# Kernel tuning notes

Hardware: AMD Instinct MI355X
Metric: run time of the kernel (lower is better)

Reference implementation:

```python
import jax, jax.numpy as jnp
import numpy as np

N_NODES, N_EDGES = 50000, 800000
IN, HID, HEADS, OUT = 128, 64, 4, 64


def _segment_softmax(e, seg, n):
    # softmax over edges grouped by source node (torch.sparse.softmax dim=1), per head
    m = jax.ops.segment_max(e, seg, num_segments=n)
    ex = jnp.exp(e - m[seg])
    s = jax.ops.segment_sum(ex, seg, num_segments=n)
    return ex / s[seg]


def _attention_layer(x, src, dst, lw, lb, aw, ab, final):
    n = x.shape[0]
    h = jax.nn.leaky_relu(x @ lw.T + lb, 0.2)            # (N, F)
    f = h.shape[1]
    # Faithful decomposition of Conv1d(2*F*H, H, k=1, groups=H) applied to
    # concat([tile(h_i, H), tile(h_j, H)]): group k covers tiled copies 2k and 2k+1;
    # copies < H come from h_i (src), copies >= H from h_j (dst).
    k = jnp.arange(HEADS)
    sel1 = (2 * k < HEADS).astype(h.dtype)[:, None]       # first half of group weights
    sel2 = (2 * k + 1 < HEADS).astype(h.dtype)[:, None]   # second half
    Wi = aw[:, :f] * sel1 + aw[:, f:] * sel2              # (H, F) acting on h_src
    Wj = aw[:, :f] * (1.0 - sel1) + aw[:, f:] * (1.0 - sel2)  # (H, F) acting on h_dst
    e = (h @ Wi.T)[src] + (h @ Wj.T)[dst] + ab            # (E, H)
    alpha = _segment_softmax(e, src, n)                   # (E, H)
    # h2[i] = sum_{j in N(i)} h[j] outer alpha[ij]  -> (N, F, H)
    h2 = jax.ops.segment_sum(h[dst][:, :, None] * alpha[:, None, :], src, num_segments=n)
    if final:
        return jax.nn.relu(h2.mean(axis=-1))              # (N, OUT)
    return jax.nn.relu(h2.reshape(n, -1))                 # (N, F*H)


def setup_inputs() -> dict:
    key = jax.random.key(0)
    ks = jax.random.split(key, 16)
    d = {}
    d["x"] = jax.random.normal(ks[0], (N_NODES, IN), jnp.float32)
    dims_in = [IN, HID * HEADS, HID * HEADS]
    dims_out = [HID, HID, OUT]
    i = 1
    for L in range(3):
        di, do = dims_in[L], dims_out[L]
        d[f"lin{L}_w"] = jax.random.normal(ks[i], (do, di), jnp.float32) / np.float32(np.sqrt(di)); i += 1
        d[f"lin{L}_b"] = jax.random.normal(ks[i], (do,), jnp.float32) * 0.01; i += 1
        d[f"att{L}_w"] = jax.random.normal(ks[i], (HEADS, 2 * do), jnp.float32) / np.float32(np.sqrt(2 * do)); i += 1
        d[f"att{L}_b"] = jax.random.normal(ks[i], (HEADS,), jnp.float32) * 0.01; i += 1
    d["src"] = jnp.sort(jax.random.randint(ks[13], (N_EDGES,), 0, N_NODES, dtype=jnp.int32))
    d["dst"] = jax.random.randint(ks[14], (N_EDGES,), 0, N_NODES, dtype=jnp.int32)
    return d


def reference(x, lin0_w, lin0_b, att0_w, att0_b, lin1_w, lin1_b, att1_w, att1_b,
              lin2_w, lin2_b, att2_w, att2_b, src, dst):
    layers = [(lin0_w, lin0_b, att0_w, att0_b),
              (lin1_w, lin1_b, att1_w, att1_b),
              (lin2_w, lin2_b, att2_w, att2_b)]
    out = x
    for i, (lw, lb, aw, ab) in enumerate(layers):
        out = _attention_layer(out, src, dst, lw, lb, aw, ab, final=(i == len(layers) - 1))
    return out
```

## Files before the change

kernel.cpp:

```cpp
#include <hip/hip_runtime.h>
#include <hip/hip_fp16.h>

#define N_NODES 50000
#define N_EDGES 800000

typedef _Float16 half8 __attribute__((ext_vector_type(8)));
typedef _Float16 f16x4 __attribute__((ext_vector_type(4)));
typedef float floatx4 __attribute__((ext_vector_type(4)));

__global__ __launch_bounds__(256) void setup_kernel(const int* __restrict__ src,
                                                    int* __restrict__ row_ptr,
                                                    const float* __restrict__ lw0,
                                                    const float* __restrict__ lw1,
                                                    const float* __restrict__ lw2,
                                                    _Float16* __restrict__ w0p,
                                                    _Float16* __restrict__ w1p,
                                                    _Float16* __restrict__ w2p) {
    int idx = blockIdx.x * 256 + threadIdx.x;
    if (blockIdx.y == 0) {
        if (idx > N_NODES) return;
        int lo = 0, hi = N_EDGES;
        while (lo < hi) {
            int mid = (lo + hi) >> 1;
            if (src[mid] < idx) lo = mid + 1; else hi = mid;
        }
        row_ptr[idx] = lo;
        return;
    }
    if (blockIdx.y == 1) {
        if (idx < 64 * 128) w0p[idx] = (_Float16)lw0[idx];
        return;
    }
    if (idx >= 64 * 192) return;
    int o = idx / 192, r = idx % 192;
    int ch = r >> 6, f = r & 63;
    const float* lw = (blockIdx.y == 2) ? lw1 : lw2;
    float v;
    if (ch == 0)      v = lw[o * 256 + f * 4 + 0] + lw[o * 256 + f * 4 + 1];
    else if (ch == 1) v = lw[o * 256 + f * 4 + 2];
    else              v = lw[o * 256 + f * 4 + 3];
    (blockIdx.y == 2 ? w1p : w2p)[idx] = (_Float16)v;
}

template <typename TIn, int K>
__global__ __launch_bounds__(256) void lin_kernel(const TIn* __restrict__ in,
                                                  const _Float16* __restrict__ w,
                                                  const float* __restrict__ b,
                                                  const float* __restrict__ aw,
                                                  _Float16* __restrict__ h,
                                                  float2* __restrict__ s, int n) {
    const int t = threadIdx.x;
    const int l = t & 63;
    const int wv = t >> 6;
    const int arow = l & 15;
    const int kg = l >> 4;
    const long rowbase = (long)blockIdx.x * 64 + wv * 16;
    long arow_g = rowbase + arow;
    if (arow_g >= n) arow_g = n - 1;

    floatx4 acc[4] = {};

    for (int kc = 0; kc < K; kc += 32) {
        const int ks = kc + kg * 8;
        half8 a;
        if (sizeof(TIn) == 4) {
            const TIn* ap = in + arow_g * K + ks;
            #pragma unroll
            for (int j = 0; j < 8; ++j) a[j] = (_Float16)ap[j];
        } else {
            a = *(const half8*)((const _Float16*)in + arow_g * K + ks);
        }
        #pragma unroll
        for (int ct = 0; ct < 4; ++ct) {
            half8 bb = *(const half8*)(w + (long)(ct * 16 + arow) * K + ks);
            acc[ct] = __builtin_amdgcn_mfma_f32_16x16x32_f16(a, bb, acc[ct], 0, 0, 0);
        }
    }

    const int c = l & 15;
    const int rq = l >> 4;
    float bias[4], a2c[4], a3c[4];
    #pragma unroll
    for (int ct = 0; ct < 4; ++ct) {
        int col = ct * 16 + c;
        bias[ct] = b[col];
        a2c[ct] = aw[2 * 128 + col] + aw[2 * 128 + 64 + col];
        a3c[ct] = aw[3 * 128 + col] + aw[3 * 128 + 64 + col];
    }
    #pragma unroll
    for (int r = 0; r < 4; ++r) {
        long row = rowbase + rq * 4 + r;
        bool ok = row < n;
        float q2 = 0.f, q3 = 0.f;
        _Float16 hv[4];
        #pragma unroll
        for (int ct = 0; ct < 4; ++ct) {
            float u = acc[ct][r] + bias[ct];
            u = u > 0.f ? u : 0.2f * u;
            q2 += u * a2c[ct];
            q3 += u * a3c[ct];
            hv[ct] = (_Float16)u;
        }
        if (ok) {
            #pragma unroll
            for (int ct = 0; ct < 4; ++ct) h[row * 64 + ct * 16 + c] = hv[ct];
        }
        #pragma unroll
        for (int o = 1; o < 16; o <<= 1) {
            q2 += __shfl_xor(q2, o);
            q3 += __shfl_xor(q3, o);
        }
        if (c == 0 && ok) s[row] = make_float2(__expf(q2), __expf(q3));
    }
}

template <int FINAL>
__global__ __launch_bounds__(256) void layer_kernel(const _Float16* __restrict__ hfeat,
                                                    const float2* __restrict__ E,
                                                    const int* __restrict__ dst,
                                                    const int* __restrict__ row_ptr,
                                                    const _Float16* __restrict__ w,
                                                    const float* __restrict__ b,
                                                    const float* __restrict__ aw,
                                                    _Float16* __restrict__ h_out,
                                                    float2* __restrict__ s_out,
                                                    float* __restrict__ out_f) {
    __shared__ _Float16 g_lds[16][200];
    __shared__ float2 spart[4][16];

    const int t = threadIdx.x;
    const int l = t & 63;
    const int wv = t >> 6;
    const int q = l >> 4;
    const int fl = l & 15;
    const int base = blockIdx.x * 16;
    const int i = base + wv * 4 + q;

    const int r0 = row_ptr[i];
    const int deg = row_ptr[i + 1] - r0;
    int md = deg;
    md = max(md, __shfl_xor(md, 16));
    md = max(md, __shfl_xor(md, 32));

    float am[4] = {}, a2[4] = {}, a3[4] = {};
    float S2 = 0.f, S3 = 0.f;
    const int safew = deg > 0 ? r0 + deg - 1 : 0;

    for (int c0 = 0; c0 < md; c0 += 16) {
        const int dl = dst[min(r0 + c0 + fl, safew)];
        const int jn = min(16, md - c0);
        for (int j = 0; j < jn; j += 4) {
            int dg[4]; float vm[4];
            #pragma unroll
            for (int g = 0; g < 4; ++g) {
                const int sl = j + g;
                dg[g] = __shfl(dl, (q << 4) | sl);
                vm[g] = (c0 + sl < deg) ? 1.f : 0.f;
            }
            f16x4 hv[4]; float2 Ev[4];
            #pragma unroll
            for (int g = 0; g < 4; ++g) {
                hv[g] = *(const f16x4*)(hfeat + (long)dg[g] * 64 + fl * 4);
                Ev[g] = E[dg[g]];
            }
            #pragma unroll
            for (int g = 0; g < 4; ++g) {
                const float e2 = vm[g] * Ev[g].x, e3 = vm[g] * Ev[g].y;
                S2 += e2; S3 += e3;
                #pragma unroll
                for (int k = 0; k < 4; ++k) {
                    const float hf = (float)hv[g][k];
                    am[k] += vm[g] * hf;
                    a2[k] += e2 * hf;
                    a3[k] += e3 * hf;
                }
            }
        }
    }

    const float inv_deg = deg > 0 ? 1.f / (float)deg : 0.f;
    const float i2 = deg > 0 ? 1.f / S2 : 0.f;
    const float i3 = deg > 0 ? 1.f / S3 : 0.f;

    if (FINAL) {
        floatx4 o;
        #pragma unroll
        for (int k = 0; k < 4; ++k)
            o[k] = fmaxf(0.5f * inv_deg * am[k] + 0.25f * (a2[k] * i2 + a3[k] * i3), 0.f);
        *(floatx4*)(out_f + (long)i * 64 + fl * 4) = o;
        return;
    }

    {
        const int nl = wv * 4 + q;
        f16x4 o0, o1, o2;
        #pragma unroll
        for (int k = 0; k < 4; ++k) {
            o0[k] = (_Float16)fmaxf(am[k] * inv_deg, 0.f);
            o1[k] = (_Float16)fmaxf(a2[k] * i2, 0.f);
            o2[k] = (_Float16)fmaxf(a3[k] * i3, 0.f);
        }
        *(f16x4*)(&g_lds[nl][fl * 4])       = o0;
        *(f16x4*)(&g_lds[nl][64 + fl * 4])  = o1;
        *(f16x4*)(&g_lds[nl][128 + fl * 4]) = o2;
    }
    __syncthreads();

    floatx4 acc = {};
    #pragma unroll
    for (int kc = 0; kc < 192; kc += 32) {
        const int ks = kc + q * 8;
        half8 a = *(const half8*)(&g_lds[fl][ks]);
        half8 bb = *(const half8*)(w + (long)(wv * 16 + fl) * 192 + ks);
        acc = __builtin_amdgcn_mfma_f32_16x16x32_f16(a, bb, acc, 0, 0, 0);
    }

    const int col = wv * 16 + fl;
    const float bias = b[col];
    const float a2c = aw[2 * 128 + col] + aw[2 * 128 + 64 + col];
    const float a3c = aw[3 * 128 + col] + aw[3 * 128 + 64 + col];
    #pragma unroll
    for (int r = 0; r < 4; ++r) {
        const int row = q * 4 + r;
        float u = acc[r] + bias;
        u = u > 0.f ? u : 0.2f * u;
        h_out[(long)(base + row) * 64 + col] = (_Float16)u;
        float q2 = u * a2c, q3 = u * a3c;
        #pragma unroll
        for (int o = 1; o < 16; o <<= 1) {
            q2 += __shfl_xor(q2, o);
            q3 += __shfl_xor(q3, o);
        }
        if (fl == 0) spart[wv][row] = make_float2(q2, q3);
    }
    __syncthreads();
    if (t < 16) {
        const float2 p0 = spart[0][t], p1 = spart[1][t], p2 = spart[2][t], p3 = spart[3][t];
        s_out[base + t] = make_float2(__expf(p0.x + p1.x + p2.x + p3.x),
                                      __expf(p0.y + p1.y + p2.y + p3.y));
    }
}

extern "C" void kernel_launch(void* const* d_in, const int* in_sizes, int n_in,
                              void* d_out, int out_size, void* d_ws, size_t ws_size,
                              hipStream_t stream) {
    const float* x = (const float*)d_in[0];
    const float* lw[3] = {(const float*)d_in[1], (const float*)d_in[5], (const float*)d_in[9]};
    const float* lb[3] = {(const float*)d_in[2], (const float*)d_in[6], (const float*)d_in[10]};
    const float* aw[3] = {(const float*)d_in[3], (const float*)d_in[7], (const float*)d_in[11]};
    const int* src = (const int*)d_in[13];
    const int* dst = (const int*)d_in[14];
    float* out = (float*)d_out;

    const int N = N_NODES;

    _Float16* hA = (_Float16*)d_ws;
    _Float16* hB = hA + (size_t)N * 64;
    float2* sA = (float2*)(hB + (size_t)N * 64);
    float2* sB = sA + N;
    _Float16* w0p = (_Float16*)(sB + N);
    _Float16* w1p = w0p + 64 * 128;
    _Float16* w2p = w1p + 64 * 192;
    int* row_ptr = (int*)(w2p + 64 * 192);

    const int lin_grid = (N + 63) / 64;
    const int layer_grid = N / 16;

    setup_kernel<<<dim3(196, 4), 256, 0, stream>>>(src, row_ptr, lw[0], lw[1], lw[2],
                                                   w0p, w1p, w2p);

    lin_kernel<float, 128><<<lin_grid, 256, 0, stream>>>(x, w0p, lb[0], aw[0], hA, sA, N);

    layer_kernel<0><<<layer_grid, 256, 0, stream>>>(hA, sA, dst, row_ptr,
                                                    w1p, lb[1], aw[1], hB, sB, out);

    layer_kernel<0><<<layer_grid, 256, 0, stream>>>(hB, sB, dst, row_ptr,
                                                    w2p, lb[2], aw[2], hA, sA, out);

    layer_kernel<1><<<layer_grid, 256, 0, stream>>>(hA, sA, dst, row_ptr,
                                                    w2p, lb[2], aw[2], hB, sB, out);
}
```

Baseline: 199.9 us.

## Fuse all stages into one cooperative persistent kernel with grid syncs

Replaces the five separate launches (setup, linear, three layer kernels) with one cooperative kernel of 768 blocks. The blocks loop over virtual blocks and use grid-wide syncs between stages, falling back to separate launches if the cooperative launch fails. The aim is to remove launch gaps and tail effects between dependent stages. In exchange, the grid is capped at 768 persistent blocks, the setup work now runs as a grid-stride loop, and grid.sync barriers cost time of their own.

```diff
diff --git a/kernel.cpp b/kernel.cpp
--- a/kernel.cpp
+++ b/kernel.cpp
@@ -1,60 +1,31 @@
 #include <hip/hip_runtime.h>
 #include <hip/hip_fp16.h>
+#include <hip/hip_cooperative_groups.h>
+
+namespace cg = cooperative_groups;
 
 #define N_NODES 50000
 #define N_EDGES 800000
+#define COOP_GRID 768
 
 typedef _Float16 half8 __attribute__((ext_vector_type(8)));
 typedef _Float16 f16x4 __attribute__((ext_vector_type(4)));
 typedef float floatx4 __attribute__((ext_vector_type(4)));
 
-__global__ __launch_bounds__(256) void setup_kernel(const int* __restrict__ src,
-                                                    int* __restrict__ row_ptr,
-                                                    const float* __restrict__ lw0,
-                                                    const float* __restrict__ lw1,
-                                                    const float* __restrict__ lw2,
-                                                    _Float16* __restrict__ w0p,
-                                                    _Float16* __restrict__ w1p,
-                                                    _Float16* __restrict__ w2p) {
-    int idx = blockIdx.x * 256 + threadIdx.x;
-    if (blockIdx.y == 0) {
-        if (idx > N_NODES) return;
-        int lo = 0, hi = N_EDGES;
-        while (lo < hi) {
-            int mid = (lo + hi) >> 1;
-            if (src[mid] < idx) lo = mid + 1; else hi = mid;
-        }
-        row_ptr[idx] = lo;
-        return;
-    }
-    if (blockIdx.y == 1) {
-        if (idx < 64 * 128) w0p[idx] = (_Float16)lw0[idx];
-        return;
-    }
-    if (idx >= 64 * 192) return;
-    int o = idx / 192, r = idx % 192;
-    int ch = r >> 6, f = r & 63;
-    const float* lw = (blockIdx.y == 2) ? lw1 : lw2;
-    float v;
-    if (ch == 0)      v = lw[o * 256 + f * 4 + 0] + lw[o * 256 + f * 4 + 1];
-    else if (ch == 1) v = lw[o * 256 + f * 4 + 2];
-    else              v = lw[o * 256 + f * 4 + 3];
-    (blockIdx.y == 2 ? w1p : w2p)[idx] = (_Float16)v;
-}
 
 template <typename TIn, int K>
-__global__ __launch_bounds__(256) void lin_kernel(const TIn* __restrict__ in,
-                                                  const _Float16* __restrict__ w,
-                                                  const float* __restrict__ b,
-                                                  const float* __restrict__ aw,
-                                                  _Float16* __restrict__ h,
-                                                  float2* __restrict__ s, int n) {
-    const int t = threadIdx.x;
+__device__ __forceinline__ void lin_body(int vb, int t,
+                                         const TIn* __restrict__ in,
+                                         const _Float16* __restrict__ w,
+                                         const float* __restrict__ b,
+                                         const float* __restrict__ aw,
+                                         _Float16* __restrict__ h,
+                                         float2* __restrict__ s, int n) {
     const int l = t & 63;
     const int wv = t >> 6;
     const int arow = l & 15;
     const int kg = l >> 4;
-    const long rowbase = (long)blockIdx.x * 64 + wv * 16;
+    const long rowbase = (long)vb * 64 + wv * 16;
     long arow_g = rowbase + arow;
     if (arow_g >= n) arow_g = n - 1;
 
@@ -112,6 +83,231 @@
         }
         if (c == 0 && ok) s[row] = make_float2(__expf(q2), __expf(q3));
     }
+}
+
+template <int FINAL>
+__device__ __forceinline__ void layer_body(int vb, int t,
+                                           const _Float16* __restrict__ hfeat,
+                                           const float2* __restrict__ E,
+                                           const int* __restrict__ dst,
+                                           const int* __restrict__ row_ptr,
+                                           const _Float16* __restrict__ w,
+                                           const float* __restrict__ b,
+                                           const float* __restrict__ aw,
+                                           _Float16* __restrict__ h_out,
+                                           float2* __restrict__ s_out,
+                                           float* __restrict__ out_f,
+                                           _Float16 (*g_lds)[200],
+                                           float2 (*spart)[16]) {
+    const int l = t & 63;
+    const int wv = t >> 6;
+    const int q = l >> 4;
+    const int fl = l & 15;
+    const int base = vb * 16;
+    const int i = base + wv * 4 + q;
+
+    const int r0 = row_ptr[i];
+    const int deg = row_ptr[i + 1] - r0;
+    int md = deg;
+    md = max(md, __shfl_xor(md, 16));
+    md = max(md, __shfl_xor(md, 32));
+
+    float am[4] = {}, a2[4] = {}, a3[4] = {};
+    float S2 = 0.f, S3 = 0.f;
+    const int safew = deg > 0 ? r0 + deg - 1 : 0;
+
+    for (int c0 = 0; c0 < md; c0 += 16) {
+        const int dl = dst[min(r0 + c0 + fl, safew)];
+        const int jn = min(16, md - c0);
+        for (int j = 0; j < jn; j += 4) {
+            int dg[4]; float vm[4];
+            #pragma unroll
+            for (int g = 0; g < 4; ++g) {
+                const int sl = j + g;
+                dg[g] = __shfl(dl, (q << 4) | sl);
+                vm[g] = (c0 + sl < deg) ? 1.f : 0.f;
+            }
+            f16x4 hv[4]; float2 Ev[4];
+            #pragma unroll
+            for (int g = 0; g < 4; ++g) {
+                hv[g] = *(const f16x4*)(hfeat + (long)dg[g] * 64 + fl * 4);
+                Ev[g] = E[dg[g]];
+            }
+            #pragma unroll
+            for (int g = 0; g < 4; ++g) {
+                const float e2 = vm[g] * Ev[g].x, e3 = vm[g] * Ev[g].y;
+                S2 += e2; S3 += e3;
+                #pragma unroll
+                for (int k = 0; k < 4; ++k) {
+                    const float hf = (float)hv[g][k];
+                    am[k] += vm[g] * hf;
+                    a2[k] += e2 * hf;
+                    a3[k] += e3 * hf;
+                }
+            }
+        }
+    }
+
+    const float inv_deg = deg > 0 ? 1.f / (float)deg : 0.f;
+    const float i2 = deg > 0 ? 1.f / S2 : 0.f;
+    const float i3 = deg > 0 ? 1.f / S3 : 0.f;
+
+    if (FINAL) {
+        floatx4 o;
+        #pragma unroll
+        for (int k = 0; k < 4; ++k)
+            o[k] = fmaxf(0.5f * inv_deg * am[k] + 0.25f * (a2[k] * i2 + a3[k] * i3), 0.f);
+        *(floatx4*)(out_f + (long)i * 64 + fl * 4) = o;
+        return;
+    }
+
+    {
+        const int nl = wv * 4 + q;
+        f16x4 o0, o1, o2;
+        #pragma unroll
+        for (int k = 0; k < 4; ++k) {
+            o0[k] = (_Float16)fmaxf(am[k] * inv_deg, 0.f);
+            o1[k] = (_Float16)fmaxf(a2[k] * i2, 0.f);
+            o2[k] = (_Float16)fmaxf(a3[k] * i3, 0.f);
+        }
+        *(f16x4*)(&g_lds[nl][fl * 4])       = o0;
+        *(f16x4*)(&g_lds[nl][64 + fl * 4])  = o1;
+        *(f16x4*)(&g_lds[nl][128 + fl * 4]) = o2;
+    }
+    __syncthreads();
+
+    floatx4 acc = {};
+    #pragma unroll
+    for (int kc = 0; kc < 192; kc += 32) {
+        const int ks = kc + q * 8;
+        half8 a = *(const half8*)(&g_lds[fl][ks]);
+        half8 bb = *(const half8*)(w + (long)(wv * 16 + fl) * 192 + ks);
+        acc = __builtin_amdgcn_mfma_f32_16x16x32_f16(a, bb, acc, 0, 0, 0);
+    }
+
+    const int col = wv * 16 + fl;
+    const float bias = b[col];
+    const float a2c = aw[2 * 128 + col] + aw[2 * 128 + 64 + col];
+    const float a3c = aw[3 * 128 + col] + aw[3 * 128 + 64 + col];
+    #pragma unroll
+    for (int r = 0; r < 4; ++r) {
+        const int row = q * 4 + r;
+        float u = acc[r] + bias;
+        u = u > 0.f ? u : 0.2f * u;
+        h_out[(long)(base + row) * 64 + col] = (_Float16)u;
+        float q2 = u * a2c, q3 = u * a3c;
+        #pragma unroll
+        for (int o = 1; o < 16; o <<= 1) {
+            q2 += __shfl_xor(q2, o);
+            q3 += __shfl_xor(q3, o);
+        }
+        if (fl == 0) spart[wv][row] = make_float2(q2, q3);
+    }
+    __syncthreads();
+    if (t < 16) {
+        const float2 p0 = spart[0][t], p1 = spart[1][t], p2 = spart[2][t], p3 = spart[3][t];
+        s_out[base + t] = make_float2(__expf(p0.x + p1.x + p2.x + p3.x),
+                                      __expf(p0.y + p1.y + p2.y + p3.y));
+    }
+}
+
+__device__ __forceinline__ void setup_body(int gid, int gstride,
+                                           const int* __restrict__ src,
+                                           int* __restrict__ row_ptr,
+                                           const float* __restrict__ lw0,
+                                           const float* __restrict__ lw1,
+                                           const float* __restrict__ lw2,
+                                           _Float16* __restrict__ w0p,
+                                           _Float16* __restrict__ w1p,
+                                           _Float16* __restrict__ w2p) {
+    for (int idx = gid; idx <= N_NODES; idx += gstride) {
+        int lo = 0, hi = N_EDGES;
+        while (lo < hi) {
+            int mid = (lo + hi) >> 1;
+            if (src[mid] < idx) lo = mid + 1; else hi = mid;
+        }
+        row_ptr[idx] = lo;
+    }
+    for (int idx = gid; idx < 64 * 128; idx += gstride) w0p[idx] = (_Float16)lw0[idx];
+    for (int idx = gid; idx < 64 * 192; idx += gstride) {
+        int o = idx / 192, r = idx % 192;
+        int ch = r >> 6, f = r & 63;
+        float v1, v2;
+        if (ch == 0) {
+            v1 = lw1[o * 256 + f * 4 + 0] + lw1[o * 256 + f * 4 + 1];
+            v2 = lw2[o * 256 + f * 4 + 0] + lw2[o * 256 + f * 4 + 1];
+        } else if (ch == 1) {
+            v1 = lw1[o * 256 + f * 4 + 2];
+            v2 = lw2[o * 256 + f * 4 + 2];
+        } else {
+            v1 = lw1[o * 256 + f * 4 + 3];
+            v2 = lw2[o * 256 + f * 4 + 3];
+        }
+        w1p[idx] = (_Float16)v1;
+        w2p[idx] = (_Float16)v2;
+    }
+}
+
+__global__ __launch_bounds__(256, 4) void fused_all(
+    const float* __restrict__ x,
+    const float* __restrict__ lw0, const float* __restrict__ lb0, const float* __restrict__ aw0,
+    const float* __restrict__ lw1, const float* __restrict__ lb1, const float* __restrict__ aw1,
+    const float* __restrict__ lw2, const float* __restrict__ lb2, const float* __restrict__ aw2,
+    const int* __restrict__ src, const int* __restrict__ dst,
+    float* __restrict__ out,
+    _Float16* __restrict__ hA, _Float16* __restrict__ hB,
+    float2* __restrict__ sA, float2* __restrict__ sB,
+    _Float16* __restrict__ w0p, _Float16* __restrict__ w1p, _Float16* __restrict__ w2p,
+    int* __restrict__ row_ptr) {
+    __shared__ _Float16 g_lds[16][200];
+    __shared__ float2 spart[4][16];
+
+    cg::grid_group grid = cg::this_grid();
+    const int t = threadIdx.x;
+    const int gs = gridDim.x;
+    const int gid = blockIdx.x * 256 + t;
+
+    setup_body(gid, gs * 256, src, row_ptr, lw0, lw1, lw2, w0p, w1p, w2p);
+    grid.sync();
+
+    const int lin_vbs = (N_NODES + 63) / 64;
+    for (int vb = blockIdx.x; vb < lin_vbs; vb += gs)
+        lin_body<float, 128>(vb, t, x, w0p, lb0, aw0, hA, sA, N_NODES);
+    grid.sync();
+
+    const int layer_vbs = N_NODES / 16;
+    for (int vb = blockIdx.x; vb < layer_vbs; vb += gs)
+        layer_body<0>(vb, t, hA, sA, dst, row_ptr, w1p, lb1, aw1, hB, sB, out, g_lds, spart);
+    grid.sync();
+
+    for (int vb = blockIdx.x; vb < layer_vbs; vb += gs)
+        layer_body<0>(vb, t, hB, sB, dst, row_ptr, w2p, lb2, aw2, hA, sA, out, g_lds, spart);
+    grid.sync();
+
+    for (int vb = blockIdx.x; vb < layer_vbs; vb += gs)
+        layer_body<1>(vb, t, hA, sA, dst, row_ptr, w2p, lb2, aw2, hB, sB, out, g_lds, spart);
+}
+
+__global__ __launch_bounds__(256) void setup_kernel(const int* __restrict__ src,
+                                                    int* __restrict__ row_ptr,
+                                                    const float* __restrict__ lw0,
+                                                    const float* __restrict__ lw1,
+                                                    const float* __restrict__ lw2,
+                                                    _Float16* __restrict__ w0p,
+                                                    _Float16* __restrict__ w1p,
+                                                    _Float16* __restrict__ w2p) {
+    setup_body(blockIdx.x * 256 + threadIdx.x, gridDim.x * 256,
+               src, row_ptr, lw0, lw1, lw2, w0p, w1p, w2p);
+}
+
+template <typename TIn, int K>
+__global__ __launch_bounds__(256) void lin_kernel(const TIn* __restrict__ in,
+                                                  const _Float16* __restrict__ w,
+                                                  const float* __restrict__ b,
+                                                  const float* __restrict__ aw,
+                                                  _Float16* __restrict__ h,
+                                                  float2* __restrict__ s, int n) {
+    lin_body<TIn, K>(blockIdx.x, threadIdx.x, in, w, b, aw, h, s, n);
 }
 
 template <int FINAL>
@@ -127,127 +323,23 @@
                                                     float* __restrict__ out_f) {
     __shared__ _Float16 g_lds[16][200];
     __shared__ float2 spart[4][16];
-
-    const int t = threadIdx.x;
-    const int l = t & 63;
-    const int wv = t >> 6;
-    const int q = l >> 4;
-    const int fl = l & 15;
-    const int base = blockIdx.x * 16;
-    const int i = base + wv * 4 + q;
-
-    const int r0 = row_ptr[i];
-    const int deg = row_ptr[i + 1] - r0;
-    int md = deg;
-    md = max(md, __shfl_xor(md, 16));
-    md = max(md, __shfl_xor(md, 32));
-
-    float am[4] = {}, a2[4] = {}, a3[4] = {};
-    float S2 = 0.f, S3 = 0.f;
-    const int safew = deg > 0 ? r0 + deg - 1 : 0;
-
-    for (int c0 = 0; c0 < md; c0 += 16) {
-        const int dl = dst[min(r0 + c0 + fl, safew)];
-        const int jn = min(16, md - c0);
-        for (int j = 0; j < jn; j += 4) {
-            int dg[4]; float vm[4];
-            #pragma unroll
-            for (int g = 0; g < 4; ++g) {
-                const int sl = j + g;
-                dg[g] = __shfl(dl, (q << 4) | sl);
-                vm[g] = (c0 + sl < deg) ? 1.f : 0.f;
-            }
-            f16x4 hv[4]; float2 Ev[4];
-            #pragma unroll
-            for (int g = 0; g < 4; ++g) {
-                hv[g] = *(const f16x4*)(hfeat + (long)dg[g] * 64 + fl * 4);
-                Ev[g] = E[dg[g]];
-            }
-            #pragma unroll
-            for (int g = 0; g < 4; ++g) {
-                const float e2 = vm[g] * Ev[g].x, e3 = vm[g] * Ev[g].y;
-                S2 += e2; S3 += e3;
-                #pragma unroll
-                for (int k = 0; k < 4; ++k) {
-                    const float hf = (float)hv[g][k];
-                    am[k] += vm[g] * hf;
-                    a2[k] += e2 * hf;
-                    a3[k] += e3 * hf;
-                }
-            }
-        }
-    }
-
-    const float inv_deg = deg > 0 ? 1.f / (float)deg : 0.f;
-    const float i2 = deg > 0 ? 1.f / S2 : 0.f;
-    const float i3 = deg > 0 ? 1.f / S3 : 0.f;
-
-    if (FINAL) {
-        floatx4 o;
-        #pragma unroll
-        for (int k = 0; k < 4; ++k)
-            o[k] = fmaxf(0.5f * inv_deg * am[k] + 0.25f * (a2[k] * i2 + a3[k] * i3), 0.f);
-        *(floatx4*)(out_f + (long)i * 64 + fl * 4) = o;
-        return;
-    }
-
-    {
-        const int nl = wv * 4 + q;
-        f16x4 o0, o1, o2;
-        #pragma unroll
-        for (int k = 0; k < 4; ++k) {
-            o0[k] = (_Float16)fmaxf(am[k] * inv_deg, 0.f);
-            o1[k] = (_Float16)fmaxf(a2[k] * i2, 0.f);
-            o2[k] = (_Float16)fmaxf(a3[k] * i3, 0.f);
-        }
-        *(f16x4*)(&g_lds[nl][fl * 4])       = o0;
-        *(f16x4*)(&g_lds[nl][64 + fl * 4])  = o1;
-        *(f16x4*)(&g_lds[nl][128 + fl * 4]) = o2;
-    }
-    __syncthreads();
-
-    floatx4 acc = {};
-    #pragma unroll
-    for (int kc = 0; kc < 192; kc += 32) {
-        const int ks = kc + q * 8;
-        half8 a = *(const half8*)(&g_lds[fl][ks]);
-        half8 bb = *(const half8*)(w + (long)(wv * 16 + fl) * 192 + ks);
-        acc = __builtin_amdgcn_mfma_f32_16x16x32_f16(a, bb, acc, 0, 0, 0);
-    }
-
-    const int col = wv * 16 + fl;
-    const float bias = b[col];
-    const float a2c = aw[2 * 128 + col] + aw[2 * 128 + 64 + col];
-    const float a3c = aw[3 * 128 + col] + aw[3 * 128 + 64 + col];
-    #pragma unroll
-    for (int r = 0; r < 4; ++r) {
-        const int row = q * 4 + r;
-        float u = acc[r] + bias;
-        u = u > 0.f ? u : 0.2f * u;
-        h_out[(long)(base + row) * 64 + col] = (_Float16)u;
-        float q2 = u * a2c, q3 = u * a3c;
-        #pragma unroll
-        for (int o = 1; o < 16; o <<= 1) {
-            q2 += __shfl_xor(q2, o);
-            q3 += __shfl_xor(q3, o);
-        }
-        if (fl == 0) spart[wv][row] = make_float2(q2, q3);
-    }
-    __syncthreads();
-    if (t < 16) {
-        const float2 p0 = spart[0][t], p1 = spart[1][t], p2 = spart[2][t], p3 = spart[3][t];
-        s_out[base + t] = make_float2(__expf(p0.x + p1.x + p2.x + p3.x),
-                                      __expf(p0.y + p1.y + p2.y + p3.y));
-    }
+    layer_body<FINAL>(blockIdx.x, threadIdx.x, hfeat, E, dst, row_ptr, w, b, aw,
+                      h_out, s_out, out_f, g_lds, spart);
 }
 
 extern "C" void kernel_launch(void* const* d_in, const int* in_sizes, int n_in,
                               void* d_out, int out_size, void* d_ws, size_t ws_size,
                               hipStream_t stream) {
     const float* x = (const float*)d_in[0];
-    const float* lw[3] = {(const float*)d_in[1], (const float*)d_in[5], (const float*)d_in[9]};
-    const float* lb[3] = {(const float*)d_in[2], (const float*)d_in[6], (const float*)d_in[10]};
-    const float* aw[3] = {(const float*)d_in[3], (const float*)d_in[7], (const float*)d_in[11]};
+    const float* lw0 = (const float*)d_in[1];
+    const float* lb0 = (const float*)d_in[2];
+    const float* aw0 = (const float*)d_in[3];
+    const float* lw1 = (const float*)d_in[5];
+    const float* lb1 = (const float*)d_in[6];
+    const float* aw1 = (const float*)d_in[7];
+    const float* lw2 = (const float*)d_in[9];
+    const float* lb2 = (const float*)d_in[10];
+    const float* aw2 = (const float*)d_in[11];
     const int* src = (const int*)d_in[13];
     const int* dst = (const int*)d_in[14];
     float* out = (float*)d_out;
@@ -263,20 +355,21 @@
     _Float16* w2p = w1p + 64 * 192;
     int* row_ptr = (int*)(w2p + 64 * 192);
 
+    void* kargs[] = {&x, &lw0, &lb0, &aw0, &lw1, &lb1, &aw1, &lw2, &lb2, &aw2,
+                     &src, &dst, &out, &hA, &hB, &sA, &sB, &w0p, &w1p, &w2p, &row_ptr};
+
+    hipError_t err = hipLaunchCooperativeKernel((const void*)fused_all,
+                                                dim3(COOP_GRID), dim3(256),
+                                                kargs, 0, stream);
+    if (err == hipSuccess) return;
+    (void)hipGetLastError();
+
     const int lin_grid = (N + 63) / 64;
     const int layer_grid = N / 16;
 
-    setup_kernel<<<dim3(196, 4), 256, 0, stream>>>(src, row_ptr, lw[0], lw[1], lw[2],
-                                                   w0p, w1p, w2p);
-
-    lin_kernel<float, 128><<<lin_grid, 256, 0, stream>>>(x, w0p, lb[0], aw[0], hA, sA, N);
-
-    layer_kernel<0><<<layer_grid, 256, 0, stream>>>(hA, sA, dst, row_ptr,
-                                                    w1p, lb[1], aw[1], hB, sB, out);
-
-    layer_kernel<0><<<layer_grid, 256, 0, stream>>>(hB, sB, dst, row_ptr,
-                                                    w2p, lb[2], aw[2], hA, sA, out);
-
-    layer_kernel<1><<<layer_grid, 256, 0, stream>>>(hA, sA, dst, row_ptr,
-                                                    w2p, lb[2], aw[2], hB, sB, out);
-}
+    setup_kernel<<<196, 256, 0, stream>>>(src, row_ptr, lw0, lw1, lw2, w0p, w1p, w2p);
+    lin_kernel<float, 128><<<lin_grid, 256, 0, stream>>>(x, w0p, lb0, aw0, hA, sA, N);
+    layer_kernel<0><<<layer_grid, 256, 0, stream>>>(hA, sA, dst, row_ptr, w1p, lb1, aw1, hB, sB, out);
+    layer_kernel<0><<<layer_grid, 256, 0, stream>>>(hB, sB, dst, row_ptr, w2p, lb2, aw2, hA, sA, out);
+    layer_kernel<1><<<layer_grid, 256, 0, stream>>>(hA, sA, dst, row_ptr, w2p, lb2, aw2, hB, sB, out);
+}
```

New measurement: 575.4 us. 2.88x slower.

## Balance edge aggregation across block threads with packed src/dst and LDS atomics

Applied to the files above, without the earlier changes.

Before, each 16-lane group handled one node and looped up to the block's maximum degree, so lanes idled on low-degree nodes. Now the block's contiguous edge range is split evenly among the 16 groups, and each group flushes partial sums into per-node LDS accumulators with atomics whenever the source node changes. Source and destination indices are packed into one 32-bit word in setup, which assumes node ids fit in 16 bits. This adds LDS atomic traffic, extra syncs and zero-initialisation in exchange for better load balance.

```diff
diff --git a/kernel.cpp b/kernel.cpp
--- a/kernel.cpp
+++ b/kernel.cpp
@@ -9,37 +9,45 @@
 typedef float floatx4 __attribute__((ext_vector_type(4)));
 
 __global__ __launch_bounds__(256) void setup_kernel(const int* __restrict__ src,
+                                                    const int* __restrict__ dst,
                                                     int* __restrict__ row_ptr,
+                                                    unsigned* __restrict__ packed,
                                                     const float* __restrict__ lw0,
                                                     const float* __restrict__ lw1,
                                                     const float* __restrict__ lw2,
                                                     _Float16* __restrict__ w0p,
                                                     _Float16* __restrict__ w1p,
                                                     _Float16* __restrict__ w2p) {
-    int idx = blockIdx.x * 256 + threadIdx.x;
-    if (blockIdx.y == 0) {
-        if (idx > N_NODES) return;
+    const int gid = blockIdx.x * 256 + threadIdx.x;
+    const int gstride = gridDim.x * 256;
+    for (int idx = gid; idx <= N_NODES; idx += gstride) {
         int lo = 0, hi = N_EDGES;
         while (lo < hi) {
             int mid = (lo + hi) >> 1;
             if (src[mid] < idx) lo = mid + 1; else hi = mid;
         }
         row_ptr[idx] = lo;
-        return;
-    }
-    if (blockIdx.y == 1) {
-        if (idx < 64 * 128) w0p[idx] = (_Float16)lw0[idx];
-        return;
-    }
-    if (idx >= 64 * 192) return;
-    int o = idx / 192, r = idx % 192;
-    int ch = r >> 6, f = r & 63;
-    const float* lw = (blockIdx.y == 2) ? lw1 : lw2;
-    float v;
-    if (ch == 0)      v = lw[o * 256 + f * 4 + 0] + lw[o * 256 + f * 4 + 1];
-    else if (ch == 1) v = lw[o * 256 + f * 4 + 2];
-    else              v = lw[o * 256 + f * 4 + 3];
-    (blockIdx.y == 2 ? w1p : w2p)[idx] = (_Float16)v;
+    }
+    for (int idx = gid; idx < N_EDGES; idx += gstride)
+        packed[idx] = (unsigned)src[idx] | ((unsigned)dst[idx] << 16);
+    for (int idx = gid; idx < 64 * 128; idx += gstride) w0p[idx] = (_Float16)lw0[idx];
+    for (int idx = gid; idx < 64 * 192; idx += gstride) {
+        int o = idx / 192, r = idx % 192;
+        int ch = r >> 6, f = r & 63;
+        float v1, v2;
+        if (ch == 0) {
+            v1 = lw1[o * 256 + f * 4 + 0] + lw1[o * 256 + f * 4 + 1];
+            v2 = lw2[o * 256 + f * 4 + 0] + lw2[o * 256 + f * 4 + 1];
+        } else if (ch == 1) {
+            v1 = lw1[o * 256 + f * 4 + 2];
+            v2 = lw2[o * 256 + f * 4 + 2];
+        } else {
+            v1 = lw1[o * 256 + f * 4 + 3];
+            v2 = lw2[o * 256 + f * 4 + 3];
+        }
+        w1p[idx] = (_Float16)v1;
+        w2p[idx] = (_Float16)v2;
+    }
 }
 
 template <typename TIn, int K>
@@ -117,7 +125,7 @@
 template <int FINAL>
 __global__ __launch_bounds__(256) void layer_kernel(const _Float16* __restrict__ hfeat,
                                                     const float2* __restrict__ E,
-                                                    const int* __restrict__ dst,
+                                                    const unsigned* __restrict__ packed,
                                                     const int* __restrict__ row_ptr,
                                                     const _Float16* __restrict__ w,
                                                     const float* __restrict__ b,
@@ -125,6 +133,9 @@
                                                     _Float16* __restrict__ h_out,
                                                     float2* __restrict__ s_out,
                                                     float* __restrict__ out_f) {
+    __shared__ float accum[16][3][64];
+    __shared__ float Ssum[16][2];
+    __shared__ int rp[17];
     __shared__ _Float16 g_lds[16][200];
     __shared__ float2 spart[4][16];
 
@@ -134,37 +145,65 @@
     const int q = l >> 4;
     const int fl = l & 15;
     const int base = blockIdx.x * 16;
-    const int i = base + wv * 4 + q;
-
-    const int r0 = row_ptr[i];
-    const int deg = row_ptr[i + 1] - r0;
-    int md = deg;
-    md = max(md, __shfl_xor(md, 16));
-    md = max(md, __shfl_xor(md, 32));
-
-    float am[4] = {}, a2[4] = {}, a3[4] = {};
-    float S2 = 0.f, S3 = 0.f;
-    const int safew = deg > 0 ? r0 + deg - 1 : 0;
-
-    for (int c0 = 0; c0 < md; c0 += 16) {
-        const int dl = dst[min(r0 + c0 + fl, safew)];
-        const int jn = min(16, md - c0);
-        for (int j = 0; j < jn; j += 4) {
-            int dg[4]; float vm[4];
+    const int qg = wv * 4 + q;
+
+    if (t < 17) rp[t] = row_ptr[base + t];
+    {
+        float* ap = (float*)accum;
+        #pragma unroll
+        for (int z = 0; z < 12; ++z) ap[t + z * 256] = 0.f;
+        if (t < 32) ((float*)Ssum)[t] = 0.f;
+    }
+    __syncthreads();
+
+    const int e_lo = rp[0];
+    const int W = rp[16] - e_lo;
+
+    if (W > 0) {
+        const int rs = e_lo + (int)(((unsigned)W * (unsigned)qg) >> 4);
+        const int re = e_lo + (int)(((unsigned)W * (unsigned)(qg + 1)) >> 4);
+        const int Lmax = (W + 15) >> 4;
+        const int ecl = (re > e_lo) ? re - 1 : e_lo;
+
+        int cn = (int)(packed[(rs < re) ? rs : ecl] & 0xffffu);
+        float am[4] = {}, a2[4] = {}, a3[4] = {};
+        float S2 = 0.f, S3 = 0.f;
+
+        for (int off = 0; off < Lmax; off += 4) {
+            unsigned pk[4]; float vm[4];
             #pragma unroll
             for (int g = 0; g < 4; ++g) {
-                const int sl = j + g;
-                dg[g] = __shfl(dl, (q << 4) | sl);
-                vm[g] = (c0 + sl < deg) ? 1.f : 0.f;
+                int ee = rs + off + g;
+                int ec = ee < re ? ee : ecl;
+                pk[g] = packed[ec];
+                vm[g] = ee < re ? 1.f : 0.f;
             }
             f16x4 hv[4]; float2 Ev[4];
             #pragma unroll
             for (int g = 0; g < 4; ++g) {
-                hv[g] = *(const f16x4*)(hfeat + (long)dg[g] * 64 + fl * 4);
-                Ev[g] = E[dg[g]];
+                const int dg = (int)(pk[g] >> 16);
+                hv[g] = *(const f16x4*)(hfeat + (long)dg * 64 + fl * 4);
+                Ev[g] = E[dg];
             }
             #pragma unroll
             for (int g = 0; g < 4; ++g) {
+                const int sg = (int)(pk[g] & 0xffffu);
+                if (vm[g] > 0.f && sg != cn) {
+                    const int cnl = cn - base;
+                    #pragma unroll
+                    for (int k = 0; k < 4; ++k) {
+                        atomicAdd(&accum[cnl][0][fl * 4 + k], am[k]);
+                        atomicAdd(&accum[cnl][1][fl * 4 + k], a2[k]);
+                        atomicAdd(&accum[cnl][2][fl * 4 + k], a3[k]);
+                        am[k] = 0.f; a2[k] = 0.f; a3[k] = 0.f;
+                    }
+                    if (fl == 0) {
+                        atomicAdd(&Ssum[cnl][0], S2);
+                        atomicAdd(&Ssum[cnl][1], S3);
+                    }
+                    S2 = 0.f; S3 = 0.f;
+                    cn = sg;
+                }
                 const float e2 = vm[g] * Ev[g].x, e3 = vm[g] * Ev[g].y;
                 S2 += e2; S3 += e3;
                 #pragma unroll
@@ -176,33 +215,53 @@
                 }
             }
         }
-    }
-
-    const float inv_deg = deg > 0 ? 1.f / (float)deg : 0.f;
-    const float i2 = deg > 0 ? 1.f / S2 : 0.f;
-    const float i3 = deg > 0 ? 1.f / S3 : 0.f;
+        {
+            const int cnl = cn - base;
+            #pragma unroll
+            for (int k = 0; k < 4; ++k) {
+                atomicAdd(&accum[cnl][0][fl * 4 + k], am[k]);
+                atomicAdd(&accum[cnl][1][fl * 4 + k], a2[k]);
+                atomicAdd(&accum[cnl][2][fl * 4 + k], a3[k]);
+            }
+            if (fl == 0) {
+                atomicAdd(&Ssum[cnl][0], S2);
+                atomicAdd(&Ssum[cnl][1], S3);
+            }
+        }
+    }
+    __syncthreads();
+
+    const int nl2 = t >> 4;
+    const int f2 = t & 15;
+    const int degn = rp[nl2 + 1] - rp[nl2];
+    const float idg = degn > 0 ? 1.f / (float)degn : 0.f;
+    const float iS2 = degn > 0 ? 1.f / Ssum[nl2][0] : 0.f;
+    const float iS3 = degn > 0 ? 1.f / Ssum[nl2][1] : 0.f;
 
     if (FINAL) {
         floatx4 o;
         #pragma unroll
-        for (int k = 0; k < 4; ++k)
-            o[k] = fmaxf(0.5f * inv_deg * am[k] + 0.25f * (a2[k] * i2 + a3[k] * i3), 0.f);
-        *(floatx4*)(out_f + (long)i * 64 + fl * 4) = o;
+        for (int k = 0; k < 4; ++k) {
+            const int f = f2 * 4 + k;
+            o[k] = fmaxf(0.5f * idg * accum[nl2][0][f] +
+                         0.25f * (accum[nl2][1][f] * iS2 + accum[nl2][2][f] * iS3), 0.f);
+        }
+        *(floatx4*)(out_f + (long)(base + nl2) * 64 + f2 * 4) = o;
         return;
     }
 
     {
-        const int nl = wv * 4 + q;
         f16x4 o0, o1, o2;
         #pragma unroll
         for (int k = 0; k < 4; ++k) {
-            o0[k] = (_Float16)fmaxf(am[k] * inv_deg, 0.f);
-            o1[k] = (_Float16)fmaxf(a2[k] * i2, 0.f);
-            o2[k] = (_Float16)fmaxf(a3[k] * i3, 0.f);
-        }
-        *(f16x4*)(&g_lds[nl][fl * 4])       = o0;
-        *(f16x4*)(&g_lds[nl][64 + fl * 4])  = o1;
-        *(f16x4*)(&g_lds[nl][128 + fl * 4]) = o2;
+            const int f = f2 * 4 + k;
+            o0[k] = (_Float16)fmaxf(accum[nl2][0][f] * idg, 0.f);
+            o1[k] = (_Float16)fmaxf(accum[nl2][1][f] * iS2, 0.f);
+            o2[k] = (_Float16)fmaxf(accum[nl2][2][f] * iS3, 0.f);
+        }
+        *(f16x4*)(&g_lds[nl2][f2 * 4])       = o0;
+        *(f16x4*)(&g_lds[nl2][64 + f2 * 4])  = o1;
+        *(f16x4*)(&g_lds[nl2][128 + f2 * 4]) = o2;
     }
     __syncthreads();
 
@@ -245,9 +304,15 @@
                               void* d_out, int out_size, void* d_ws, size_t ws_size,
                               hipStream_t stream) {
     const float* x = (const float*)d_in[0];
-    const float* lw[3] = {(const float*)d_in[1], (const float*)d_in[5], (const float*)d_in[9]};
-    const float* lb[3] = {(const float*)d_in[2], (const float*)d_in[6], (const float*)d_in[10]};
-    const float* aw[3] = {(const float*)d_in[3], (const float*)d_in[7], (const float*)d_in[11]};
+    const float* lw0 = (const float*)d_in[1];
+    const float* lb0 = (const float*)d_in[2];
+    const float* aw0 = (const float*)d_in[3];
+    const float* lw1 = (const float*)d_in[5];
+    const float* lb1 = (const float*)d_in[6];
+    const float* aw1 = (const float*)d_in[7];
+    const float* lw2 = (const float*)d_in[9];
+    const float* lb2 = (const float*)d_in[10];
+    const float* aw2 = (const float*)d_in[11];
     const int* src = (const int*)d_in[13];
     const int* dst = (const int*)d_in[14];
     float* out = (float*)d_out;
@@ -262,21 +327,18 @@
     _Float16* w1p = w0p + 64 * 128;
     _Float16* w2p = w1p + 64 * 192;
     int* row_ptr = (int*)(w2p + 64 * 192);
+    unsigned* packed = (unsigned*)(row_ptr + N + 1);
 
     const int lin_grid = (N + 63) / 64;
     const int layer_grid = N / 16;
 
-    setup_kernel<<<dim3(196, 4), 256, 0, stream>>>(src, row_ptr, lw[0], lw[1], lw[2],
-                                                   w0p, w1p, w2p);
-
-    lin_kernel<float, 128><<<lin_grid, 256, 0, stream>>>(x, w0p, lb[0], aw[0], hA, sA, N);
-
-    layer_kernel<0><<<layer_grid, 256, 0, stream>>>(hA, sA, dst, row_ptr,
-                                                    w1p, lb[1], aw[1], hB, sB, out);
-
-    layer_kernel<0><<<layer_grid, 256, 0, stream>>>(hB, sB, dst, row_ptr,
-                                                    w2p, lb[2], aw[2], hA, sA, out);
-
-    layer_kernel<1><<<layer_grid, 256, 0, stream>>>(hA, sA, dst, row_ptr,
-                                                    w2p, lb[2], aw[2], hB, sB, out);
+    setup_kernel<<<196, 256, 0, stream>>>(src, dst, row_ptr, packed,
+                                          lw0, lw1, lw2, w0p, w1p, w2p);
+    lin_kernel<float, 128><<<lin_grid, 256, 0, stream>>>(x, w0p, lb0, aw0, hA, sA, N);
+    layer_kernel<0><<<layer_grid, 256, 0, stream>>>(hA, sA, packed, row_ptr,
+                                                    w1p, lb1, aw1, hB, sB, out);
+    layer_kernel<0><<<layer_grid, 256, 0, stream>>>(hB, sB, packed, row_ptr,
+                                                    w2p, lb2, aw2, hA, sA, out);
+    layer_kernel<1><<<layer_grid, 256, 0, stream>>>(hA, sA, packed, row_ptr,
+                                                    w2p, lb2, aw2, hB, sB, out);
 }
```

Measured after the change: 442.5 us. +121.3%, slower.

## Partition each node's edge list by destination half to localize gathers

Applied to the files above, without the earlier changes.

Setup now reorders each node's destination list into two buckets, destinations below and above the midpoint node, and records the split point. The layer kernel walks the two buckets in an order alternated by block parity, so concurrent blocks tend to gather from the same half of the feature table. The aim is better cache locality for the random gathers. In exchange, setup does extra binary searches and a serial per-node scatter, each bucket is padded to multiples of 16 separately so more lanes sit idle, and the floating-point summation order changes.

```diff
diff --git a/kernel.cpp b/kernel.cpp
--- a/kernel.cpp
+++ b/kernel.cpp
@@ -3,43 +3,61 @@
 
 #define N_NODES 50000
 #define N_EDGES 800000
+#define BUCKET_SPLIT 25000
 
 typedef _Float16 half8 __attribute__((ext_vector_type(8)));
 typedef _Float16 f16x4 __attribute__((ext_vector_type(4)));
 typedef float floatx4 __attribute__((ext_vector_type(4)));
 
 __global__ __launch_bounds__(256) void setup_kernel(const int* __restrict__ src,
+                                                    const int* __restrict__ dst,
                                                     int* __restrict__ row_ptr,
+                                                    int* __restrict__ row_mid,
+                                                    int* __restrict__ dstp,
                                                     const float* __restrict__ lw0,
                                                     const float* __restrict__ lw1,
                                                     const float* __restrict__ lw2,
                                                     _Float16* __restrict__ w0p,
                                                     _Float16* __restrict__ w1p,
                                                     _Float16* __restrict__ w2p) {
-    int idx = blockIdx.x * 256 + threadIdx.x;
-    if (blockIdx.y == 0) {
-        if (idx > N_NODES) return;
+    const int gid = blockIdx.x * 256 + threadIdx.x;
+    const int gstride = gridDim.x * 256;
+    for (int idx = gid; idx <= N_NODES; idx += gstride) {
         int lo = 0, hi = N_EDGES;
         while (lo < hi) {
             int mid = (lo + hi) >> 1;
             if (src[mid] < idx) lo = mid + 1; else hi = mid;
         }
         row_ptr[idx] = lo;
-        return;
-    }
-    if (blockIdx.y == 1) {
-        if (idx < 64 * 128) w0p[idx] = (_Float16)lw0[idx];
-        return;
-    }
-    if (idx >= 64 * 192) return;
-    int o = idx / 192, r = idx % 192;
-    int ch = r >> 6, f = r & 63;
-    const float* lw = (blockIdx.y == 2) ? lw1 : lw2;
-    float v;
-    if (ch == 0)      v = lw[o * 256 + f * 4 + 0] + lw[o * 256 + f * 4 + 1];
-    else if (ch == 1) v = lw[o * 256 + f * 4 + 2];
-    else              v = lw[o * 256 + f * 4 + 3];
-    (blockIdx.y == 2 ? w1p : w2p)[idx] = (_Float16)v;
+    }
+    for (int i = gid; i < N_NODES; i += gstride) {
+        int lo = 0, hi = N_EDGES;
+        while (lo < hi) { int m = (lo + hi) >> 1; if (src[m] < i) lo = m + 1; else hi = m; }
+        int lo1 = lo, hi1 = N_EDGES;
+        while (lo1 < hi1) { int m = (lo1 + hi1) >> 1; if (src[m] < i + 1) lo1 = m + 1; else hi1 = m; }
+        int c = lo;
+        for (int e = lo; e < lo1; ++e) { int d = dst[e]; if (d < BUCKET_SPLIT) dstp[c++] = d; }
+        row_mid[i] = c;
+        for (int e = lo; e < lo1; ++e) { int d = dst[e]; if (d >= BUCKET_SPLIT) dstp[c++] = d; }
+    }
+    for (int idx = gid; idx < 64 * 128; idx += gstride) w0p[idx] = (_Float16)lw0[idx];
+    for (int idx = gid; idx < 64 * 192; idx += gstride) {
+        int o = idx / 192, r = idx % 192;
+        int ch = r >> 6, f = r & 63;
+        float v1, v2;
+        if (ch == 0) {
+            v1 = lw1[o * 256 + f * 4 + 0] + lw1[o * 256 + f * 4 + 1];
+            v2 = lw2[o * 256 + f * 4 + 0] + lw2[o * 256 + f * 4 + 1];
+        } else if (ch == 1) {
+            v1 = lw1[o * 256 + f * 4 + 2];
+            v2 = lw2[o * 256 + f * 4 + 2];
+        } else {
+            v1 = lw1[o * 256 + f * 4 + 3];
+            v2 = lw2[o * 256 + f * 4 + 3];
+        }
+        w1p[idx] = (_Float16)v1;
+        w2p[idx] = (_Float16)v2;
+    }
 }
 
 template <typename TIn, int K>
@@ -117,8 +135,9 @@
 template <int FINAL>
 __global__ __launch_bounds__(256) void layer_kernel(const _Float16* __restrict__ hfeat,
                                                     const float2* __restrict__ E,
-                                                    const int* __restrict__ dst,
+                                                    const int* __restrict__ dstp,
                                                     const int* __restrict__ row_ptr,
+                                                    const int* __restrict__ row_mid,
                                                     const _Float16* __restrict__ w,
                                                     const float* __restrict__ b,
                                                     const float* __restrict__ aw,
@@ -136,43 +155,51 @@
     const int base = blockIdx.x * 16;
     const int i = base + wv * 4 + q;
 
-    const int r0 = row_ptr[i];
-    const int deg = row_ptr[i + 1] - r0;
-    int md = deg;
-    md = max(md, __shfl_xor(md, 16));
-    md = max(md, __shfl_xor(md, 32));
+    const int r0 = row_ptr[i], r1 = row_ptr[i + 1], rm = row_mid[i];
+    const int deg = r1 - r0;
 
     float am[4] = {}, a2[4] = {}, a3[4] = {};
     float S2 = 0.f, S3 = 0.f;
-    const int safew = deg > 0 ? r0 + deg - 1 : 0;
-
-    for (int c0 = 0; c0 < md; c0 += 16) {
-        const int dl = dst[min(r0 + c0 + fl, safew)];
-        const int jn = min(16, md - c0);
-        for (int j = 0; j < jn; j += 4) {
-            int dg[4]; float vm[4];
-            #pragma unroll
-            for (int g = 0; g < 4; ++g) {
-                const int sl = j + g;
-                dg[g] = __shfl(dl, (q << 4) | sl);
-                vm[g] = (c0 + sl < deg) ? 1.f : 0.f;
-            }
-            f16x4 hv[4]; float2 Ev[4];
-            #pragma unroll
-            for (int g = 0; g < 4; ++g) {
-                hv[g] = *(const f16x4*)(hfeat + (long)dg[g] * 64 + fl * 4);
-                Ev[g] = E[dg[g]];
-            }
-            #pragma unroll
-            for (int g = 0; g < 4; ++g) {
-                const float e2 = vm[g] * Ev[g].x, e3 = vm[g] * Ev[g].y;
-                S2 += e2; S3 += e3;
+
+    #pragma unroll
+    for (int pp = 0; pp < 2; ++pp) {
+        const int p = pp ^ (int)(blockIdx.x & 1);
+        const int plo = p ? rm : r0;
+        const int phi = p ? r1 : rm;
+        const int pdeg = phi - plo;
+        int md = pdeg;
+        md = max(md, __shfl_xor(md, 16));
+        md = max(md, __shfl_xor(md, 32));
+        const int psafe = pdeg > 0 ? phi - 1 : 0;
+
+        for (int c0 = 0; c0 < md; c0 += 16) {
+            const int dl = dstp[min(plo + c0 + fl, psafe)];
+            const int jn = min(16, md - c0);
+            for (int j = 0; j < jn; j += 4) {
+                int dg[4]; float vm[4];
                 #pragma unroll
-                for (int k = 0; k < 4; ++k) {
-                    const float hf = (float)hv[g][k];
-                    am[k] += vm[g] * hf;
-                    a2[k] += e2 * hf;
-                    a3[k] += e3 * hf;
+                for (int g = 0; g < 4; ++g) {
+                    const int sl = j + g;
+                    dg[g] = __shfl(dl, (q << 4) | sl);
+                    vm[g] = (c0 + sl < pdeg) ? 1.f : 0.f;
+                }
+                f16x4 hv[4]; float2 Ev[4];
+                #pragma unroll
+                for (int g = 0; g < 4; ++g) {
+                    hv[g] = *(const f16x4*)(hfeat + (long)dg[g] * 64 + fl * 4);
+                    Ev[g] = E[dg[g]];
+                }
+                #pragma unroll
+                for (int g = 0; g < 4; ++g) {
+                    const float e2 = vm[g] * Ev[g].x, e3 = vm[g] * Ev[g].y;
+                    S2 += e2; S3 += e3;
+                    #pragma unroll
+                    for (int k = 0; k < 4; ++k) {
+                        const float hf = (float)hv[g][k];
+                        am[k] += vm[g] * hf;
+                        a2[k] += e2 * hf;
+                        a3[k] += e3 * hf;
+                    }
                 }
             }
         }
@@ -245,9 +272,15 @@
                               void* d_out, int out_size, void* d_ws, size_t ws_size,
                               hipStream_t stream) {
     const float* x = (const float*)d_in[0];
-    const float* lw[3] = {(const float*)d_in[1], (const float*)d_in[5], (const float*)d_in[9]};
-    const float* lb[3] = {(const float*)d_in[2], (const float*)d_in[6], (const float*)d_in[10]};
-    const float* aw[3] = {(const float*)d_in[3], (const float*)d_in[7], (const float*)d_in[11]};
+    const float* lw0 = (const float*)d_in[1];
+    const float* lb0 = (const float*)d_in[2];
+    const float* aw0 = (const float*)d_in[3];
+    const float* lw1 = (const float*)d_in[5];
+    const float* lb1 = (const float*)d_in[6];
+    const float* aw1 = (const float*)d_in[7];
+    const float* lw2 = (const float*)d_in[9];
+    const float* lb2 = (const float*)d_in[10];
+    const float* aw2 = (const float*)d_in[11];
     const int* src = (const int*)d_in[13];
     const int* dst = (const int*)d_in[14];
     float* out = (float*)d_out;
@@ -262,21 +295,19 @@
     _Float16* w1p = w0p + 64 * 128;
     _Float16* w2p = w1p + 64 * 192;
     int* row_ptr = (int*)(w2p + 64 * 192);
+    int* row_mid = row_ptr + N + 1;
+    int* dstp = row_mid + N;
 
     const int lin_grid = (N + 63) / 64;
     const int layer_grid = N / 16;
 
-    setup_kernel<<<dim3(196, 4), 256, 0, stream>>>(src, row_ptr, lw[0], lw[1], lw[2],
-                                                   w0p, w1p, w2p);
-
-    lin_kernel<float, 128><<<lin_grid, 256, 0, stream>>>(x, w0p, lb[0], aw[0], hA, sA, N);
-
-    layer_kernel<0><<<layer_grid, 256, 0, stream>>>(hA, sA, dst, row_ptr,
-                                                    w1p, lb[1], aw[1], hB, sB, out);
-
-    layer_kernel<0><<<layer_grid, 256, 0, stream>>>(hB, sB, dst, row_ptr,
-                                                    w2p, lb[2], aw[2], hA, sA, out);
-
-    layer_kernel<1><<<layer_grid, 256, 0, stream>>>(hA, sA, dst, row_ptr,
-                                                    w2p, lb[2], aw[2], hB, sB, out);
+    setup_kernel<<<196, 256, 0, stream>>>(src, dst, row_ptr, row_mid, dstp,
+                                          lw0, lw1, lw2, w0p, w1p, w2p);
+    lin_kernel<float, 128><<<lin_grid, 256, 0, stream>>>(x, w0p, lb0, aw0, hA, sA, N);
+    layer_kernel<0><<<layer_grid, 256, 0, stream>>>(hA, sA, dstp, row_ptr, row_mid,
+                                                    w1p, lb1, aw1, hB, sB, out);
+    layer_kernel<0><<<layer_grid, 256, 0, stream>>>(hB, sB, dstp, row_ptr, row_mid,
+                                                    w2p, lb2, aw2, hA, sA, out);
+    layer_kernel<1><<<layer_grid, 256, 0, stream>>>(hA, sA, dstp, row_ptr, row_mid,
+                                                    w2p, lb2, aw2, hB, sB, out);
 }
```

Result: slower. 233.1 us (+16.6%).
